# Kernel optimization log

Hardware: AMD Instinct MI355X
Metric: run time of the kernel (lower is better)

## Reference

```python
import jax, jax.numpy as jnp
import numpy as np


def graph_conv(x, W, b, src, dst, n_nodes):
    """DGL GraphConv, norm='both', activation=relu.
    Pre-scale by out-degree^-1/2 of src, project (in>out so project first),
    sum-aggregate over edges, post-scale by in-degree^-1/2 of dst."""
    ones = jnp.ones(src.shape[0], dtype=x.dtype)
    deg_out = jax.ops.segment_sum(ones, src, num_segments=n_nodes)
    deg_in = jax.ops.segment_sum(ones, dst, num_segments=n_nodes)
    norm_src = jnp.clip(deg_out, 1.0, None) ** -0.5  # [N]
    norm_dst = jnp.clip(deg_in, 1.0, None) ** -0.5   # [N]
    h = x * norm_src[:, None]
    h = h @ W  # project first since in_feats > out_feats
    # message passing: gather src features, scatter-add into dst
    agg = jax.ops.segment_sum(h[src], dst, num_segments=n_nodes)  # [N, out]
    agg = agg * norm_dst[:, None]
    return jax.nn.relu(agg + b)


def setup_inputs() -> dict:
    key = jax.random.key(0)
    ks = jax.random.split(key, 6)
    N, E, D_IN, D_HID = 50000, 800000, 1024, 256
    x = jax.random.normal(ks[0], (N, D_IN), dtype=jnp.float32)
    src = jax.random.randint(ks[1], (E,), 0, N)
    dst = jax.random.randint(ks[2], (E,), 0, N)
    # Glorot-style init for weights
    W1 = jax.random.normal(ks[3], (D_IN, D_HID), dtype=jnp.float32) * (1.0 / np.sqrt(D_IN))
    b1 = jnp.zeros((D_HID,), dtype=jnp.float32)
    W2 = jax.random.normal(ks[4], (D_HID, 1), dtype=jnp.float32) * (1.0 / np.sqrt(D_HID))
    b2 = jnp.zeros((1,), dtype=jnp.float32)
    return {"x": x, "src": src, "dst": dst, "W1": W1, "b1": b1, "W2": W2, "b2": b2, "n_nodes": N}


def reference(x, src, dst, W1, b1, W2, b2, n_nodes):
    h = graph_conv(x, W1, b1, src, dst, n_nodes)   # [N, 256]
    out = graph_conv(h, W2, b2, src, dst, n_nodes)  # [N, 1]
    return out
```

## Files before the change

kernel.cpp:

```cpp
#include <hip/hip_runtime.h>
#include <hip/hip_bf16.h>

typedef __attribute__((ext_vector_type(8))) short bf16x8;
typedef __attribute__((ext_vector_type(4))) float f32x4;

static __device__ __forceinline__ short f2bf(float f) {
    unsigned u = __float_as_uint(f);
    unsigned r = (u + 0x7FFFu + ((u >> 16) & 1u)) >> 16;
    return (short)(unsigned short)r;
}
static __device__ __forceinline__ float bf2f(short s) {
    return __uint_as_float(((unsigned)(unsigned short)s) << 16);
}

static __device__ __forceinline__ void gload16(const void* g, void* l) {
    __builtin_amdgcn_global_load_lds((const __attribute__((address_space(1))) unsigned int*)g,
                                     (__attribute__((address_space(3))) unsigned int*)l, 16, 0, 0);
}

static __device__ __forceinline__ void wg_barrier() {
    asm volatile("" ::: "memory");
    __builtin_amdgcn_s_barrier();
    asm volatile("" ::: "memory");
}

static __device__ __forceinline__ bf16x8 cvt8(const f32x4 lo, const f32x4 hi) {
    __hip_bfloat162 p0 = __float22bfloat162_rn(make_float2(lo[0], lo[1]));
    __hip_bfloat162 p1 = __float22bfloat162_rn(make_float2(lo[2], lo[3]));
    __hip_bfloat162 p2 = __float22bfloat162_rn(make_float2(hi[0], hi[1]));
    __hip_bfloat162 p3 = __float22bfloat162_rn(make_float2(hi[2], hi[3]));
    short2 s0 = *(short2*)&p0, s1 = *(short2*)&p1, s2 = *(short2*)&p2, s3 = *(short2*)&p3;
    bf16x8 r = {s0.x, s0.y, s1.x, s1.y, s2.x, s2.y, s3.x, s3.y};
    return r;
}

__global__ void deg_kernel(const int* __restrict__ src, const int* __restrict__ dst,
                           int* __restrict__ deg_out, int* __restrict__ deg_in, int E) {
    int e = blockIdx.x * blockDim.x + threadIdx.x;
    if (e < E) {
        atomicAdd(&deg_out[src[e]], 1);
        atomicAdd(&deg_in[dst[e]], 1);
    }
}

__global__ void scan_part1(const int* __restrict__ deg, int* __restrict__ bsum, int N) {
    __shared__ int red[256];
    int i = blockIdx.x * 256 + threadIdx.x;
    red[threadIdx.x] = (i < N) ? deg[i] : 0;
    __syncthreads();
    for (int off = 128; off > 0; off >>= 1) {
        if (threadIdx.x < off) red[threadIdx.x] += red[threadIdx.x + off];
        __syncthreads();
    }
    if (threadIdx.x == 0) bsum[blockIdx.x] = red[0];
}

__global__ void scan_part2(const int* __restrict__ bsum, int* __restrict__ bsum_ex, int NB,
                           int* __restrict__ offsets, int N, int E) {
    __shared__ int s[256];
    int t = threadIdx.x;
    int v = (t < NB) ? bsum[t] : 0;
    s[t] = v;
    __syncthreads();
    for (int off = 1; off < 256; off <<= 1) {
        int u = (t >= off) ? s[t - off] : 0;
        __syncthreads();
        s[t] += u;
        __syncthreads();
    }
    bsum_ex[t] = s[t] - v;
    if (t == 0) offsets[N] = E;
}

__global__ void scan_part3(const int* __restrict__ deg_in, const int* __restrict__ deg_out,
                           const int* __restrict__ bsum_ex, int* __restrict__ offsets,
                           float* __restrict__ ns, float* __restrict__ nd, int N) {
    __shared__ int s[256];
    int t = threadIdx.x, i = blockIdx.x * 256 + t;
    int v = (i < N) ? deg_in[i] : 0;
    s[t] = v;
    __syncthreads();
    for (int off = 1; off < 256; off <<= 1) {
        int u = (t >= off) ? s[t - off] : 0;
        __syncthreads();
        s[t] += u;
        __syncthreads();
    }
    if (i < N) {
        offsets[i] = bsum_ex[blockIdx.x] + s[t] - v;
        ns[i] = rsqrtf((float)max(deg_out[i], 1));
        nd[i] = rsqrtf((float)max(v, 1));
    }
}

__global__ void scatter_kernel(const int* __restrict__ src, const int* __restrict__ dst,
                               const int* __restrict__ offsets, int* __restrict__ cursor,
                               int* __restrict__ bucket, int E) {
    int e = blockIdx.x * blockDim.x + threadIdx.x;
    if (e < E) {
        int d = dst[e];
        int p = atomicAdd(&cursor[d], 1);
        bucket[offsets[d] + p] = src[e];
    }
}

__global__ __launch_bounds__(1024) void transpose_w1(const float* __restrict__ W1,
                                                     short* __restrict__ Wt) {
    __shared__ short tile[32][33];
    int k0 = blockIdx.x * 32, n0 = blockIdx.y * 32;
    int tx = threadIdx.x & 31, ty = threadIdx.x >> 5;
    tile[ty][tx] = f2bf(W1[(size_t)(k0 + ty) * 256 + (n0 + tx)]);
    __syncthreads();
    Wt[(size_t)(n0 + ty) * 1024 + (k0 + tx)] = tile[tx][ty];
}

#define BM 128
#define BN 256
#define BK 32
#define NKT 32
#define CSTR 264

union SMem {
    struct {
        float A[2][BM * BK];
        short B[2][BN * BK];
    } s;
    short C[BM * CSTR];
};

__global__ __launch_bounds__(256, 2) void gemm1_kernel(const float* __restrict__ x,
                                                       const short* __restrict__ Wt,
                                                       const float* __restrict__ norm_src,
                                                       short* __restrict__ hb, int M) {
    __shared__ __align__(16) SMem sm;
    __shared__ float ns_lds[BM];
    const int tid  = threadIdx.x;
    const int lane = tid & 63;
    const int wave = tid >> 6;
    const int quad = lane >> 4;
    const int mrow = lane & 15;
    const int wm = (wave >> 1) * 64;
    const int wn = (wave & 1) * 128;
    const int bm = blockIdx.x * BM;

    if (tid < BM) ns_lds[tid] = norm_src[min(bm + tid, M - 1)];

    f32x4 acc[4][8] = {};

    const int aL_r = lane >> 3;
    const int aL_c = (lane & 7) ^ (aL_r & 7);
    const int bL_r = lane >> 2;
    const int bL_c = (lane & 3) ^ ((lane >> 3) & 3);

    auto stageAB = [&](int buf, int k0) {
#pragma unroll
        for (int i = 0; i < 4; i++) {
            int rowbase = wave * 32 + i * 8;
            int r = min(bm + rowbase + aL_r, M - 1);
            gload16(x + (size_t)r * 1024 + k0 + aL_c * 4, &sm.s.A[buf][rowbase * 32]);
        }
#pragma unroll
        for (int i = 0; i < 4; i++) {
            int nbase = wave * 64 + i * 16;
            int n = nbase + bL_r;
            gload16(Wt + (size_t)n * 1024 + k0 + bL_c * 8, &sm.s.B[buf][nbase * 32]);
        }
    };

    stageAB(0, 0);
    stageAB(1, BK);
    asm volatile("s_waitcnt vmcnt(8)" ::: "memory");
    wg_barrier();

    int cur = 0;
    for (int t = 0; t < NKT; t++) {
        bf16x8 af[4], bfr[8];
#pragma unroll
        for (int mi = 0; mi < 4; mi++) {
            int row = wm + mi * 16 + mrow;
            f32x4 lo = *(const f32x4*)&sm.s.A[cur][row * 32 + (((quad * 2 + 0) ^ (mrow & 7)) * 4)];
            f32x4 hi = *(const f32x4*)&sm.s.A[cur][row * 32 + (((quad * 2 + 1) ^ (mrow & 7)) * 4)];
            af[mi] = cvt8(lo, hi);
        }
#pragma unroll
        for (int ni = 0; ni < 8; ni++) {
            int n = wn + ni * 16 + mrow;
            bfr[ni] = *(const bf16x8*)&sm.s.B[cur][n * 32 + ((quad ^ ((mrow >> 1) & 3)) * 8)];
        }
#pragma unroll
        for (int mi = 0; mi < 4; mi++)
#pragma unroll
            for (int ni = 0; ni < 8; ni++)
                acc[mi][ni] = __builtin_amdgcn_mfma_f32_16x16x32_bf16(af[mi], bfr[ni], acc[mi][ni], 0, 0, 0);

        wg_barrier();

        if (t + 2 < NKT) {
            stageAB(cur, (t + 2) * BK);
            asm volatile("s_waitcnt vmcnt(8)" ::: "memory");
        } else {
            asm volatile("s_waitcnt vmcnt(0)" ::: "memory");
        }
        wg_barrier();
        cur ^= 1;
    }

#pragma unroll
    for (int mi = 0; mi < 4; mi++) {
#pragma unroll
        for (int reg = 0; reg < 4; reg++) {
            int row = wm + mi * 16 + quad * 4 + reg;
            float nsv = ns_lds[row];
#pragma unroll
            for (int ni = 0; ni < 8; ni++) {
                int col = wn + ni * 16 + mrow;
                sm.C[row * CSTR + col] = f2bf(acc[mi][ni][reg] * nsv);
            }
        }
    }
    __syncthreads();
#pragma unroll
    for (int j = 0; j < 16; j++) {
        int row = wave * 2 + (lane >> 5) + j * 8;
        int chunk = lane & 31;
        if (bm + row < M) {
            int4 v = *(const int4*)&sm.C[row * CSTR + chunk * 8];
            *(int4*)(hb + (size_t)(bm + row) * 256 + chunk * 8) = v;
        }
    }
}

__global__ __launch_bounds__(256) void agg1_kernel(const short* __restrict__ hb,
                                                   const int* __restrict__ bucket,
                                                   const int* __restrict__ offsets,
                                                   const float* __restrict__ norm_dst,
                                                   const float* __restrict__ norm_src,
                                                   const float* __restrict__ b1,
                                                   const float* __restrict__ W2,
                                                   float* __restrict__ z, int N) {
    int wave = threadIdx.x >> 6;
    int lane = threadIdx.x & 63;
    int half = lane >> 5;
    int col8 = lane & 31;
    int node = blockIdx.x * 4 + wave;
    if (node >= N) return;
    int beg = offsets[node], end = offsets[node + 1];
    float a[8] = {0.f, 0.f, 0.f, 0.f, 0.f, 0.f, 0.f, 0.f};
    int e = beg;
    for (; e + 16 <= end; e += 16) {
        bf16x8 v[8];
#pragma unroll
        for (int i = 0; i < 8; i++) {
            int s = bucket[e + 2 * i + half];
            v[i] = *(const bf16x8*)(hb + (size_t)s * 256 + col8 * 8);
        }
#pragma unroll
        for (int i = 0; i < 8; i++)
#pragma unroll
            for (int j = 0; j < 8; j++) a[j] += bf2f(v[i][j]);
    }
    for (; e + 8 <= end; e += 8) {
        bf16x8 v[4];
#pragma unroll
        for (int i = 0; i < 4; i++) {
            int s = bucket[e + 2 * i + half];
            v[i] = *(const bf16x8*)(hb + (size_t)s * 256 + col8 * 8);
        }
#pragma unroll
        for (int i = 0; i < 4; i++)
#pragma unroll
            for (int j = 0; j < 8; j++) a[j] += bf2f(v[i][j]);
    }
    for (; e + 2 <= end; e += 2) {
        int s0 = bucket[e + half];
        bf16x8 v0 = *(const bf16x8*)(hb + (size_t)s0 * 256 + col8 * 8);
#pragma unroll
        for (int j = 0; j < 8; j++) a[j] += bf2f(v0[j]);
    }
    if (e < end && half == 0) {
        int s0 = bucket[e];
        bf16x8 v0 = *(const bf16x8*)(hb + (size_t)s0 * 256 + col8 * 8);
#pragma unroll
        for (int j = 0; j < 8; j++) a[j] += bf2f(v0[j]);
    }
#pragma unroll
    for (int j = 0; j < 8; j++) a[j] += __shfl_xor(a[j], 32, 64);

    float nd = norm_dst[node];
    float4 b_lo = *(const float4*)(b1 + col8 * 8);
    float4 b_hi = *(const float4*)(b1 + col8 * 8 + 4);
    float4 w_lo = *(const float4*)(W2 + col8 * 8);
    float4 w_hi = *(const float4*)(W2 + col8 * 8 + 4);
    float p = 0.f;
    p += fmaxf(a[0] * nd + b_lo.x, 0.f) * w_lo.x;
    p += fmaxf(a[1] * nd + b_lo.y, 0.f) * w_lo.y;
    p += fmaxf(a[2] * nd + b_lo.z, 0.f) * w_lo.z;
    p += fmaxf(a[3] * nd + b_lo.w, 0.f) * w_lo.w;
    p += fmaxf(a[4] * nd + b_hi.x, 0.f) * w_hi.x;
    p += fmaxf(a[5] * nd + b_hi.y, 0.f) * w_hi.y;
    p += fmaxf(a[6] * nd + b_hi.z, 0.f) * w_hi.z;
    p += fmaxf(a[7] * nd + b_hi.w, 0.f) * w_hi.w;
#pragma unroll
    for (int off = 16; off > 0; off >>= 1) p += __shfl_xor(p, off, 64);
    if (lane == 0) z[node] = p * norm_src[node];
}

__global__ void agg2_kernel(const float* __restrict__ z, const int* __restrict__ bucket,
                            const int* __restrict__ offsets, const float* __restrict__ norm_dst,
                            const float* __restrict__ b2, float* __restrict__ out, int N) {
    int i = blockIdx.x * blockDim.x + threadIdx.x;
    if (i >= N) return;
    int beg = offsets[i], end = offsets[i + 1];
    float s = 0.f;
    for (int e = beg; e < end; e++) s += z[bucket[e]];
    out[i] = fmaxf(s * norm_dst[i] + b2[0], 0.f);
}

extern "C" void kernel_launch(void* const* d_in, const int* in_sizes, int n_in,
                              void* d_out, int out_size, void* d_ws, size_t ws_size,
                              hipStream_t stream) {
    const int D_HID = in_sizes[4];
    const int D_IN  = in_sizes[3] / D_HID;
    const int N     = in_sizes[0] / D_IN;
    const int E     = in_sizes[1];

    const float* x   = (const float*)d_in[0];
    const int*   src = (const int*)d_in[1];
    const int*   dst = (const int*)d_in[2];
    const float* W1  = (const float*)d_in[3];
    const float* b1  = (const float*)d_in[4];
    const float* W2  = (const float*)d_in[5];
    const float* b2  = (const float*)d_in[6];
    float* out = (float*)d_out;

    char* p = (char*)d_ws;
    auto alloc = [&](size_t bytes) {
        void* r = (void*)p;
        p += (bytes + 255) & ~(size_t)255;
        return r;
    };
    int*   deg_out  = (int*)alloc((size_t)N * 4);
    int*   deg_in   = (int*)alloc((size_t)N * 4);
    int*   cursor   = (int*)alloc((size_t)N * 4);
    float* norm_src = (float*)alloc((size_t)N * 4);
    float* norm_dst = (float*)alloc((size_t)N * 4);
    int*   offsets  = (int*)alloc((size_t)(N + 1) * 4);
    int*   bucket   = (int*)alloc((size_t)E * 4);
    short* Wt       = (short*)alloc((size_t)D_IN * D_HID * 2);
    short* hb       = (short*)alloc((size_t)N * D_HID * 2);
    float* z        = (float*)alloc((size_t)N * 4);
    int*   bsum     = (int*)alloc(256 * 4);
    int*   bsum_ex  = (int*)alloc(256 * 4);

    const int NB = (N + 255) / 256;

    size_t degpad = ((size_t)N * 4 + 255) & ~(size_t)255;
    hipMemsetAsync(deg_out, 0, degpad * 2 + (size_t)N * 4, stream);

    deg_kernel<<<(E + 255) / 256, 256, 0, stream>>>(src, dst, deg_out, deg_in, E);
    scan_part1<<<NB, 256, 0, stream>>>(deg_in, bsum, N);
    scan_part2<<<1, 256, 0, stream>>>(bsum, bsum_ex, NB, offsets, N, E);
    scan_part3<<<NB, 256, 0, stream>>>(deg_in, deg_out, bsum_ex, offsets, norm_src, norm_dst, N);
    scatter_kernel<<<(E + 255) / 256, 256, 0, stream>>>(src, dst, offsets, cursor, bucket, E);
    transpose_w1<<<dim3(D_IN / 32, D_HID / 32), 1024, 0, stream>>>(W1, Wt);
    gemm1_kernel<<<dim3((N + BM - 1) / BM), 256, 0, stream>>>(x, Wt, norm_src, hb, N);
    agg1_kernel<<<(N + 3) / 4, 256, 0, stream>>>(hb, bucket, offsets, norm_dst, norm_src, b1, W2, z, N);
    agg2_kernel<<<(N + 255) / 256, 256, 0, stream>>>(z, bucket, offsets, norm_dst, b2, out, N);
}
```

Before: 489.4 us.

## Fuse graph preprocessing and W1 transpose into one cooperative persistent kernel

Replaces the memset, degree count, three-stage scan, CSR scatter and W1 transpose/bf16 conversion with a single cooperative kernel of 1024 blocks that uses grid-wide syncs between phases. This removes about six kernel launches and the memset, which is meant to cut launch overhead and the idle gaps between small kernels. The scan becomes per-block chunks of about 49 nodes, each serially prefix-summed by one thread, plus a one-block scan of the block sums. The cost is five grid barriers. The design also needs all 1024 blocks to be co-resident, and assumes N/1024 is at most 256 and that bsum holds 1024 entries.

```diff
diff --git a/kernel.cpp b/kernel.cpp
--- a/kernel.cpp
+++ b/kernel.cpp
@@ -1,5 +1,8 @@
 #include <hip/hip_runtime.h>
 #include <hip/hip_bf16.h>
+#include <hip/hip_cooperative_groups.h>
+
+namespace cg = cooperative_groups;
 
 typedef __attribute__((ext_vector_type(8))) short bf16x8;
 typedef __attribute__((ext_vector_type(4))) float f32x4;
@@ -34,84 +37,106 @@
     return r;
 }
 
-__global__ void deg_kernel(const int* __restrict__ src, const int* __restrict__ dst,
-                           int* __restrict__ deg_out, int* __restrict__ deg_in, int E) {
-    int e = blockIdx.x * blockDim.x + threadIdx.x;
-    if (e < E) {
+#define PREP_NB 1024
+
+__global__ __launch_bounds__(256) void prep_kernel(
+    const float* __restrict__ W1, short* __restrict__ Wt,
+    const int* __restrict__ src, const int* __restrict__ dst,
+    int* __restrict__ deg_out, int* __restrict__ deg_in, int* __restrict__ cursor,
+    float* __restrict__ ns, float* __restrict__ nd,
+    int* __restrict__ offsets, int* __restrict__ bucket, int* __restrict__ bsum,
+    int N, int E) {
+    cg::grid_group grid = cg::this_grid();
+    const int tid = threadIdx.x;
+    const int bid = blockIdx.x;
+    const int nb  = gridDim.x;
+    const int gid = bid * 256 + tid;
+    const int gstride = nb * 256;
+
+    __shared__ short tile[32][33];
+    __shared__ int sred[256];
+
+    for (int i = gid; i < N; i += gstride) { deg_out[i] = 0; deg_in[i] = 0; cursor[i] = 0; }
+    if (bid < 256) {
+        int k0 = (bid & 31) * 32, n0 = (bid >> 5) * 32;
+        int tx = tid & 31, ty = tid >> 5;
+#pragma unroll
+        for (int p = 0; p < 4; p++) {
+            int r = p * 8 + ty;
+            tile[r][tx] = f2bf(W1[(size_t)(k0 + r) * 256 + (n0 + tx)]);
+        }
+        __syncthreads();
+#pragma unroll
+        for (int p = 0; p < 4; p++) {
+            int r = p * 8 + ty;
+            Wt[(size_t)(n0 + r) * 1024 + (k0 + tx)] = tile[tx][r];
+        }
+    }
+    grid.sync();
+
+    for (int e = gid; e < E; e += gstride) {
         atomicAdd(&deg_out[src[e]], 1);
         atomicAdd(&deg_in[dst[e]], 1);
     }
-}
-
-__global__ void scan_part1(const int* __restrict__ deg, int* __restrict__ bsum, int N) {
-    __shared__ int red[256];
-    int i = blockIdx.x * 256 + threadIdx.x;
-    red[threadIdx.x] = (i < N) ? deg[i] : 0;
+    grid.sync();
+
+    const int C = (N + nb - 1) / nb;
+    const int i0 = bid * C;
+    const int cnt = max(0, min(N - i0, C));
+    sred[tid] = (tid < cnt) ? deg_in[i0 + tid] : 0;
     __syncthreads();
     for (int off = 128; off > 0; off >>= 1) {
-        if (threadIdx.x < off) red[threadIdx.x] += red[threadIdx.x + off];
+        if (tid < off) sred[tid] += sred[tid + off];
         __syncthreads();
     }
-    if (threadIdx.x == 0) bsum[blockIdx.x] = red[0];
-}
-
-__global__ void scan_part2(const int* __restrict__ bsum, int* __restrict__ bsum_ex, int NB,
-                           int* __restrict__ offsets, int N, int E) {
-    __shared__ int s[256];
-    int t = threadIdx.x;
-    int v = (t < NB) ? bsum[t] : 0;
-    s[t] = v;
+    if (tid == 0) bsum[bid] = sred[0];
+    grid.sync();
+
+    if (bid == 0) {
+        int p0 = bsum[tid * 4 + 0], p1 = bsum[tid * 4 + 1];
+        int p2 = bsum[tid * 4 + 2], p3 = bsum[tid * 4 + 3];
+        int lsum = p0 + p1 + p2 + p3;
+        sred[tid] = lsum;
+        __syncthreads();
+        for (int off = 1; off < 256; off <<= 1) {
+            int u = (tid >= off) ? sred[tid - off] : 0;
+            __syncthreads();
+            sred[tid] += u;
+            __syncthreads();
+        }
+        int base = sred[tid] - lsum;
+        bsum[tid * 4 + 0] = base;
+        bsum[tid * 4 + 1] = base + p0;
+        bsum[tid * 4 + 2] = base + p0 + p1;
+        bsum[tid * 4 + 3] = base + p0 + p1 + p2;
+    }
+    grid.sync();
+
+    if (tid < cnt) sred[tid] = deg_in[i0 + tid];
     __syncthreads();
-    for (int off = 1; off < 256; off <<= 1) {
-        int u = (t >= off) ? s[t - off] : 0;
-        __syncthreads();
-        s[t] += u;
-        __syncthreads();
-    }
-    bsum_ex[t] = s[t] - v;
-    if (t == 0) offsets[N] = E;
-}
-
-__global__ void scan_part3(const int* __restrict__ deg_in, const int* __restrict__ deg_out,
-                           const int* __restrict__ bsum_ex, int* __restrict__ offsets,
-                           float* __restrict__ ns, float* __restrict__ nd, int N) {
-    __shared__ int s[256];
-    int t = threadIdx.x, i = blockIdx.x * 256 + t;
-    int v = (i < N) ? deg_in[i] : 0;
-    s[t] = v;
+    if (tid == 0 && cnt > 0) {
+        int run = bsum[bid];
+        for (int j = 0; j < cnt; j++) {
+            int d = sred[j];
+            sred[j] = run;
+            run += d;
+        }
+    }
     __syncthreads();
-    for (int off = 1; off < 256; off <<= 1) {
-        int u = (t >= off) ? s[t - off] : 0;
-        __syncthreads();
-        s[t] += u;
-        __syncthreads();
-    }
-    if (i < N) {
-        offsets[i] = bsum_ex[blockIdx.x] + s[t] - v;
+    if (tid < cnt) {
+        int i = i0 + tid;
+        offsets[i] = sred[tid];
         ns[i] = rsqrtf((float)max(deg_out[i], 1));
-        nd[i] = rsqrtf((float)max(v, 1));
-    }
-}
-
-__global__ void scatter_kernel(const int* __restrict__ src, const int* __restrict__ dst,
-                               const int* __restrict__ offsets, int* __restrict__ cursor,
-                               int* __restrict__ bucket, int E) {
-    int e = blockIdx.x * blockDim.x + threadIdx.x;
-    if (e < E) {
+        nd[i] = rsqrtf((float)max(deg_in[i], 1));
+    }
+    if (gid == 0) offsets[N] = E;
+    grid.sync();
+
+    for (int e = gid; e < E; e += gstride) {
         int d = dst[e];
         int p = atomicAdd(&cursor[d], 1);
         bucket[offsets[d] + p] = src[e];
     }
-}
-
-__global__ __launch_bounds__(1024) void transpose_w1(const float* __restrict__ W1,
-                                                     short* __restrict__ Wt) {
-    __shared__ short tile[32][33];
-    int k0 = blockIdx.x * 32, n0 = blockIdx.y * 32;
-    int tx = threadIdx.x & 31, ty = threadIdx.x >> 5;
-    tile[ty][tx] = f2bf(W1[(size_t)(k0 + ty) * 256 + (n0 + tx)]);
-    __syncthreads();
-    Wt[(size_t)(n0 + ty) * 1024 + (k0 + tx)] = tile[tx][ty];
 }
 
 #define BM 128
@@ -321,8 +346,8 @@
                               hipStream_t stream) {
     const int D_HID = in_sizes[4];
     const int D_IN  = in_sizes[3] / D_HID;
-    const int N     = in_sizes[0] / D_IN;
-    const int E     = in_sizes[1];
+    int N = in_sizes[0] / D_IN;
+    int E = in_sizes[1];
 
     const float* x   = (const float*)d_in[0];
     const int*   src = (const int*)d_in[1];
@@ -349,20 +374,15 @@
     short* Wt       = (short*)alloc((size_t)D_IN * D_HID * 2);
     short* hb       = (short*)alloc((size_t)N * D_HID * 2);
     float* z        = (float*)alloc((size_t)N * 4);
-    int*   bsum     = (int*)alloc(256 * 4);
-    int*   bsum_ex  = (int*)alloc(256 * 4);
-
-    const int NB = (N + 255) / 256;
-
-    size_t degpad = ((size_t)N * 4 + 255) & ~(size_t)255;
-    hipMemsetAsync(deg_out, 0, degpad * 2 + (size_t)N * 4, stream);
-
-    deg_kernel<<<(E + 255) / 256, 256, 0, stream>>>(src, dst, deg_out, deg_in, E);
-    scan_part1<<<NB, 256, 0, stream>>>(deg_in, bsum, N);
-    scan_part2<<<1, 256, 0, stream>>>(bsum, bsum_ex, NB, offsets, N, E);
-    scan_part3<<<NB, 256, 0, stream>>>(deg_in, deg_out, bsum_ex, offsets, norm_src, norm_dst, N);
-    scatter_kernel<<<(E + 255) / 256, 256, 0, stream>>>(src, dst, offsets, cursor, bucket, E);
-    transpose_w1<<<dim3(D_IN / 32, D_HID / 32), 1024, 0, stream>>>(W1, Wt);
+    int*   bsum     = (int*)alloc(PREP_NB * 4);
+
+    void* args[] = {(void*)&W1, (void*)&Wt, (void*)&src, (void*)&dst,
+                    (void*)&deg_out, (void*)&deg_in, (void*)&cursor,
+                    (void*)&norm_src, (void*)&norm_dst,
+                    (void*)&offsets, (void*)&bucket, (void*)&bsum,
+                    (void*)&N, (void*)&E};
+    hipLaunchCooperativeKernel((void*)prep_kernel, dim3(PREP_NB), dim3(256), args, 0, stream);
+
     gemm1_kernel<<<dim3((N + BM - 1) / BM), 256, 0, stream>>>(x, Wt, norm_src, hb, N);
     agg1_kernel<<<(N + 3) / 4, 256, 0, stream>>>(hb, bucket, offsets, norm_dst, norm_src, b1, W2, z, N);
     agg2_kernel<<<(N + 255) / 256, 256, 0, stream>>>(z, bucket, offsets, norm_dst, b2, out, N);
```

After: 1.041 ms. 2.13x slower.

## Fuse W1 transpose into degree kernel and CSR scatter into GEMM launch

Applied to the files above, without the earlier changes.

The W1 transpose now runs as extra blocks of the degree-counting kernel. The degree atomic on dst also records each edge's rank, which removes the separate cursor array and the atomics in the scatter pass. The scatter then runs as extra non-GEMM blocks appended to the GEMM launch. This cuts two kernel launches and a pass of atomics, at the cost of an E-sized rank buffer and scatter blocks competing with GEMM blocks for CUs.

```diff
diff --git a/kernel.cpp b/kernel.cpp
--- a/kernel.cpp
+++ b/kernel.cpp
@@ -34,12 +34,35 @@
     return r;
 }
 
-__global__ void deg_kernel(const int* __restrict__ src, const int* __restrict__ dst,
-                           int* __restrict__ deg_out, int* __restrict__ deg_in, int E) {
-    int e = blockIdx.x * blockDim.x + threadIdx.x;
-    if (e < E) {
-        atomicAdd(&deg_out[src[e]], 1);
-        atomicAdd(&deg_in[dst[e]], 1);
+__global__ __launch_bounds__(256) void deg_tr_kernel(const float* __restrict__ W1,
+                                                     short* __restrict__ Wt,
+                                                     const int* __restrict__ src,
+                                                     const int* __restrict__ dst,
+                                                     int* __restrict__ deg_out,
+                                                     int* __restrict__ deg_in,
+                                                     int* __restrict__ rank, int E) {
+    int bid = blockIdx.x, tid = threadIdx.x;
+    if (bid < 256) {
+        __shared__ short tile[32][33];
+        int k0 = (bid & 31) * 32, n0 = (bid >> 5) * 32;
+        int tx = tid & 31, ty = tid >> 5;
+#pragma unroll
+        for (int p = 0; p < 4; p++) {
+            int r = p * 8 + ty;
+            tile[r][tx] = f2bf(W1[(size_t)(k0 + r) * 256 + (n0 + tx)]);
+        }
+        __syncthreads();
+#pragma unroll
+        for (int p = 0; p < 4; p++) {
+            int r = p * 8 + ty;
+            Wt[(size_t)(n0 + r) * 1024 + (k0 + tx)] = tile[tx][r];
+        }
+    } else {
+        int e = (bid - 256) * 256 + tid;
+        if (e < E) {
+            atomicAdd(&deg_out[src[e]], 1);
+            rank[e] = atomicAdd(&deg_in[dst[e]], 1);
+        }
     }
 }
 
@@ -93,32 +116,12 @@
     }
 }
 
-__global__ void scatter_kernel(const int* __restrict__ src, const int* __restrict__ dst,
-                               const int* __restrict__ offsets, int* __restrict__ cursor,
-                               int* __restrict__ bucket, int E) {
-    int e = blockIdx.x * blockDim.x + threadIdx.x;
-    if (e < E) {
-        int d = dst[e];
-        int p = atomicAdd(&cursor[d], 1);
-        bucket[offsets[d] + p] = src[e];
-    }
-}
-
-__global__ __launch_bounds__(1024) void transpose_w1(const float* __restrict__ W1,
-                                                     short* __restrict__ Wt) {
-    __shared__ short tile[32][33];
-    int k0 = blockIdx.x * 32, n0 = blockIdx.y * 32;
-    int tx = threadIdx.x & 31, ty = threadIdx.x >> 5;
-    tile[ty][tx] = f2bf(W1[(size_t)(k0 + ty) * 256 + (n0 + tx)]);
-    __syncthreads();
-    Wt[(size_t)(n0 + ty) * 1024 + (k0 + tx)] = tile[tx][ty];
-}
-
 #define BM 128
 #define BN 256
 #define BK 32
 #define NKT 32
 #define CSTR 264
+#define SCB 782
 
 union SMem {
     struct {
@@ -128,12 +131,23 @@
     short C[BM * CSTR];
 };
 
-__global__ __launch_bounds__(256, 2) void gemm1_kernel(const float* __restrict__ x,
-                                                       const short* __restrict__ Wt,
-                                                       const float* __restrict__ norm_src,
-                                                       short* __restrict__ hb, int M) {
+__global__ __launch_bounds__(256, 2) void gemm_scatter_kernel(
+    const float* __restrict__ x, const short* __restrict__ Wt,
+    const float* __restrict__ norm_src, short* __restrict__ hb, int M,
+    const int* __restrict__ src, const int* __restrict__ dst,
+    const int* __restrict__ offsets, const int* __restrict__ rank,
+    int* __restrict__ bucket, int E, int GB) {
     __shared__ __align__(16) SMem sm;
     __shared__ float ns_lds[BM];
+
+    if ((int)blockIdx.x >= GB) {
+        int base = ((int)blockIdx.x - GB) * 256 + threadIdx.x;
+        for (int e = base; e < E; e += SCB * 256) {
+            bucket[offsets[dst[e]] + rank[e]] = src[e];
+        }
+        return;
+    }
+
     const int tid  = threadIdx.x;
     const int lane = tid & 63;
     const int wave = tid >> 6;
@@ -341,10 +355,10 @@
     };
     int*   deg_out  = (int*)alloc((size_t)N * 4);
     int*   deg_in   = (int*)alloc((size_t)N * 4);
-    int*   cursor   = (int*)alloc((size_t)N * 4);
     float* norm_src = (float*)alloc((size_t)N * 4);
     float* norm_dst = (float*)alloc((size_t)N * 4);
     int*   offsets  = (int*)alloc((size_t)(N + 1) * 4);
+    int*   rank     = (int*)alloc((size_t)E * 4);
     int*   bucket   = (int*)alloc((size_t)E * 4);
     short* Wt       = (short*)alloc((size_t)D_IN * D_HID * 2);
     short* hb       = (short*)alloc((size_t)N * D_HID * 2);
@@ -353,17 +367,17 @@
     int*   bsum_ex  = (int*)alloc(256 * 4);
 
     const int NB = (N + 255) / 256;
+    const int GB = (N + BM - 1) / BM;
 
     size_t degpad = ((size_t)N * 4 + 255) & ~(size_t)255;
-    hipMemsetAsync(deg_out, 0, degpad * 2 + (size_t)N * 4, stream);
-
-    deg_kernel<<<(E + 255) / 256, 256, 0, stream>>>(src, dst, deg_out, deg_in, E);
+    hipMemsetAsync(deg_out, 0, degpad + (size_t)N * 4, stream);
+
+    deg_tr_kernel<<<256 + (E + 255) / 256, 256, 0, stream>>>(W1, Wt, src, dst, deg_out, deg_in, rank, E);
     scan_part1<<<NB, 256, 0, stream>>>(deg_in, bsum, N);
     scan_part2<<<1, 256, 0, stream>>>(bsum, bsum_ex, NB, offsets, N, E);
     scan_part3<<<NB, 256, 0, stream>>>(deg_in, deg_out, bsum_ex, offsets, norm_src, norm_dst, N);
-    scatter_kernel<<<(E + 255) / 256, 256, 0, stream>>>(src, dst, offsets, cursor, bucket, E);
-    transpose_w1<<<dim3(D_IN / 32, D_HID / 32), 1024, 0, stream>>>(W1, Wt);
-    gemm1_kernel<<<dim3((N + BM - 1) / BM), 256, 0, stream>>>(x, Wt, norm_src, hb, N);
+    gemm_scatter_kernel<<<GB + SCB, 256, 0, stream>>>(x, Wt, norm_src, hb, N,
+                                                      src, dst, offsets, rank, bucket, E, GB);
     agg1_kernel<<<(N + 3) / 4, 256, 0, stream>>>(hb, bucket, offsets, norm_dst, norm_src, b1, W2, z, N);
     agg2_kernel<<<(N + 255) / 256, 256, 0, stream>>>(z, bucket, offsets, norm_dst, b2, out, N);
 }
```

New measurement: 468.1 us. 4.4% less time.
